# Kernel tuning notes

Hardware: AMD Instinct MI355X
Metric: run time of the kernel (lower is better)

The kernel has to match this reference:

```python
import jax, jax.numpy as jnp
import numpy as np

THRESHOLD = 0.5
N_SEG = 5
NEG_INF = -1e30
EPS = 1e-12  # F.normalize eps


def setup_inputs() -> dict:
    key = jax.random.key(0)
    kx, kl = jax.random.split(key)
    B, D, L = 4096, 512, 80
    x = jax.random.normal(kx, (B, D), dtype=jnp.float32)
    labels = jax.random.randint(kl, (B, L), 0, 2, dtype=jnp.int32)
    return {"x": x, "labels": labels}


def reference(x, labels):
    B = x.shape[0]
    labels_f = labels.astype(jnp.float32)
    # pairwise Jaccard over multi-hot labels
    intersection = labels_f @ labels_f.T                      # [B, B]
    counts = labels_f.sum(axis=1, keepdims=True)              # [B, 1]
    union = counts + counts.T - intersection
    jaccard = intersection / union                            # [B, B]
    # cosine similarity (F.normalize with eps clamp)
    norm = jnp.maximum(jnp.linalg.norm(x, axis=1, keepdims=True), EPS)
    nx = x / norm
    sim = nx @ nx.T                                           # [B, B]
    # --- sample positive (uniform among jaccard > threshold), fixed key ---
    pos_mask = jaccard > THRESHOLD
    valid_mask = jnp.any(pos_mask, axis=1)                    # [B]
    logits = jnp.where(pos_mask, 0.0, NEG_INF)
    sampled = jax.random.categorical(jax.random.key(42), logits, axis=-1)
    pos_samples = jnp.where(valid_mask, sampled, 0)           # invalid rows -> 0
    # --- top-k negatives: jaccard strictly below the positive's jaccard ---
    pos_sim_j = jaccard[jnp.arange(B), pos_samples]           # [B]
    neg_mask = jaccard < pos_sim_j[:, None]
    neg_sims = jnp.where(neg_mask, jaccard, -jnp.inf)
    _, neg_samples = jax.lax.top_k(neg_sims, N_SEG)           # [B, N_SEG]
    # --- contrastive loss on cosine sims at sampled indices ---
    rel_pos = sim[jnp.arange(B), pos_samples]                 # [B]
    rel_neg = jnp.take_along_axis(sim, neg_samples, axis=1)   # [B, N_SEG]
    exp_pos = jnp.exp(rel_pos)
    sum_exp_neg = jnp.exp(rel_neg).sum(axis=1)
    loss = -jnp.log(exp_pos / (exp_pos + sum_exp_neg))
    vm = valid_mask.astype(x.dtype)
    return (loss * vm).sum() / vm.sum()
```

## Files before the change

### kernel.cpp

```cpp
#include <hip/hip_runtime.h>
#include <stdint.h>

#define B_ROWS 4096
#define DIMS   512
#define NLAB   80
#define HALF_ROWS 2048
#define HCNT   8388608u
#define CHUNK  1024
#define SCAP   1024

typedef unsigned long long u64;

__device__ __forceinline__ uint32_t rotl32(uint32_t x, uint32_t d) {
    return (x << d) | (x >> (32u - d));
}

__device__ __forceinline__ void tf2x32_key42(uint32_t c0, uint32_t c1,
                                             uint32_t& o0, uint32_t& o1) {
    const uint32_t ks0 = 0u;
    const uint32_t ks1 = 42u;
    const uint32_t ks2 = 0x1BD11BDAu ^ 0u ^ 42u;
    uint32_t x0 = c0 + ks0;
    uint32_t x1 = c1 + ks1;
#define TF_RND(r) { x0 += x1; x1 = rotl32(x1, (r)); x1 ^= x0; }
    TF_RND(13u) TF_RND(15u) TF_RND(26u) TF_RND(6u)
    x0 += ks1; x1 += ks2 + 1u;
    TF_RND(17u) TF_RND(29u) TF_RND(16u) TF_RND(24u)
    x0 += ks2; x1 += ks0 + 2u;
    TF_RND(13u) TF_RND(15u) TF_RND(26u) TF_RND(6u)
    x0 += ks0; x1 += ks1 + 3u;
    TF_RND(17u) TF_RND(29u) TF_RND(16u) TF_RND(24u)
    x0 += ks1; x1 += ks2 + 4u;
    TF_RND(13u) TF_RND(15u) TF_RND(26u) TF_RND(6u)
    x0 += ks2; x1 += ks0 + 5u;
#undef TF_RND
    o0 = x0; o1 = x1;
}

__device__ __forceinline__ u64 shflx64(u64 v, int m) {
    uint32_t lo = __shfl_xor((uint32_t)(v & 0xFFFFFFFFull), m, 64);
    uint32_t hi = __shfl_xor((uint32_t)(v >> 32), m, 64);
    return ((u64)hi << 32) | (u64)lo;
}

__device__ __forceinline__ uint32_t umx(uint32_t a, uint32_t b) { return a > b ? a : b; }
__device__ __forceinline__ uint32_t umn(uint32_t a, uint32_t b) { return a < b ? a : b; }

__device__ __forceinline__ void ins5_u32(uint32_t* t, uint32_t k) {
    t[4] = umx(t[4], k);
    uint32_t hi, lo;
    hi = umx(t[3], t[4]); lo = umn(t[3], t[4]); t[3] = hi; t[4] = lo;
    hi = umx(t[2], t[3]); lo = umn(t[2], t[3]); t[2] = hi; t[3] = lo;
    hi = umx(t[1], t[2]); lo = umn(t[1], t[2]); t[1] = hi; t[2] = lo;
    hi = umx(t[0], t[1]); lo = umn(t[0], t[1]); t[0] = hi; t[1] = lo;
}

__device__ __forceinline__ void merge5_u32(uint32_t* A, const uint32_t* Bv) {
    uint32_t a0=A[0],a1=A[1],a2=A[2],a3=A[3],a4=A[4];
    uint32_t b0=Bv[0],b1=Bv[1],b2=Bv[2],b3=Bv[3],b4=Bv[4];
    uint32_t m0 = umx(a0, b0);
    uint32_t m1 = umx(umx(a1, b1), umn(a0, b0));
    uint32_t m2 = umx(umx(a2, b2), umx(umn(a0, b1), umn(a1, b0)));
    uint32_t m3 = umx(umx(a3, b3), umx(umx(umn(a0, b2), umn(a1, b1)), umn(a2, b0)));
    uint32_t m4 = umx(umx(a4, b4), umx(umx(umn(a0, b3), umn(a1, b2)),
                                       umx(umn(a2, b1), umn(a3, b0))));
    A[0]=m0; A[1]=m1; A[2]=m2; A[3]=m3; A[4]=m4;
}

__device__ __forceinline__ uint32_t jkey19(uint32_t it, uint32_t u) {
    const uint32_t n = it << 19;
    float f = (float)it * __builtin_amdgcn_rcpf((float)u) * 524288.0f;
    uint32_t ak = (uint32_t)f;
    int r = (int)(n - ak * u);
    if (r < 0) { ak--; r += (int)u; }
    if (r >= (int)u) ak++;
    return ak + 1u;
}


__global__ __launch_bounds__(256) void prep_kernel(const int* __restrict__ labels,
                                                   uint4* __restrict__ pk,
                                                   uint32_t* __restrict__ scnt) {
    const int tid = threadIdx.x;
    const int lane = tid & 63;
    const int row = blockIdx.x * 4 + (tid >> 6);
    const int* lr = labels + (size_t)row * NLAB;
    const int la = lr[lane];
    const int lb = (lane < 16) ? lr[64 + lane] : 0;
    const u64 b0 = __ballot(la != 0);
    const u64 b1 = __ballot(lb != 0);
    const uint32_t w2 = (uint32_t)b1 & 0xFFFFu;
    const uint32_t cnt = (uint32_t)__popcll(b0) + (uint32_t)__popc(w2);
    if (lane == 0) {
        pk[row] = make_uint4((uint32_t)b0, (uint32_t)(b0 >> 32), w2, cnt);
        scnt[row] = 0u;
    }
}

__global__ __launch_bounds__(256) void scan_kernel(const uint4* __restrict__ pk,
                                                   uint32_t* __restrict__ scnt,
                                                   uint32_t* __restrict__ sList,
                                                   uint32_t* __restrict__ keys5P) {
    __shared__ uint4 tab[CHUNK];
    const int tid = threadIdx.x;
    const int grp = (int)blockIdx.x >> 2;
    const int sub = (int)blockIdx.x & 3;
    const int jbase = sub * CHUNK;
#pragma unroll
    for (int k = 0; k < 4; ++k) tab[tid + 256 * k] = pk[jbase + tid + 256 * k];
    __syncthreads();

    const int lane = tid & 63;
    const int pr = grp * 4 + (tid >> 6);
    const int r0 = pr, r1 = pr + HALF_ROWS;
    const uint4 P0 = pk[r0], P1 = pk[r1];
    const uint32_t cw0 = P0.w, cw1 = P1.w;

    uint32_t t0[5], t1[5];
#pragma unroll
    for (int k = 0; k < 5; ++k) {
        const uint32_t fk = (uint32_t)(~(jbase + k)) & 0xFFFu;
        t0[k] = fk; t1[k] = fk;
    }

#pragma unroll 4
    for (int jb = 0; jb < CHUNK; jb += 64) {
        const int jl = jb + lane;
        const int j  = jbase + jl;
        const uint4 pj = tab[jl];
        const uint32_t cj = pj.w;
        const uint32_t jx = (~(uint32_t)j) & 0xFFFu;
        const uint32_t it0 = (uint32_t)(__popc(P0.x & pj.x) + __popc(P0.y & pj.y) + __popc(P0.z & pj.z));
        const uint32_t u0  = cw0 + cj - it0;
        const uint32_t it1 = (uint32_t)(__popc(P1.x & pj.x) + __popc(P1.y & pj.y) + __popc(P1.z & pj.z));
        const uint32_t u1  = cw1 + cj - it1;
        const bool c0 = (it0 << 1) > u0;
        const bool c1 = (it1 << 1) > u1;
        if (__any(c0 || c1)) {
            if (c0) {
                uint32_t slot = atomicAdd(&scnt[r0], 1u);
                if (slot < SCAP) sList[((uint32_t)r0 << 10) + slot] = (it0 << 20) | (u0 << 12) | (uint32_t)j;
            }
            if (c1) {
                uint32_t slot = atomicAdd(&scnt[r1], 1u);
                if (slot < SCAP) sList[((uint32_t)r1 << 10) + slot] = (it1 << 20) | (u1 << 12) | (uint32_t)j;
            }
        }
        if (!c0) {
            const uint32_t thr = umx(t0[4] >> 12, 1u) - 1u;
            if ((it0 << 19) >= __umul24(thr, u0))
                ins5_u32(t0, (jkey19(it0, u0) << 12) | jx);
        }
        if (!c1) {
            const uint32_t thr = umx(t1[4] >> 12, 1u) - 1u;
            if ((it1 << 19) >= __umul24(thr, u1))
                ins5_u32(t1, (jkey19(it1, u1) << 12) | jx);
        }
    }
#pragma unroll
    for (int m = 1; m < 64; m <<= 1) {
        uint32_t o[5];
#pragma unroll
        for (int k = 0; k < 5; ++k) o[k] = __shfl_xor(t0[k], m, 64);
        merge5_u32(t0, o);
#pragma unroll
        for (int k = 0; k < 5; ++k) o[k] = __shfl_xor(t1[k], m, 64);
        merge5_u32(t1, o);
    }
    if (lane == 0) {
        const int idx = (pr << 2) | sub;
#pragma unroll
        for (int k = 0; k < 5; ++k) {
            keys5P[idx * 10 + k]     = t0[k];
            keys5P[idx * 10 + 5 + k] = t1[k];
        }
    }
}

__global__ __launch_bounds__(256) void fin_kernel(const float* __restrict__ x,
                                                  const uint32_t* __restrict__ scnt,
                                                  const uint32_t* __restrict__ sList,
                                                  const uint32_t* __restrict__ keys5P,
                                                  float2* __restrict__ blockPart) {
    __shared__ float lossW[4], cntW[4];
    const int tid = threadIdx.x;
    const int lane = tid & 63;
    const int w = tid >> 6;
    const int row = (int)blockIdx.x * 4 + w;
    const int pr   = row & (HALF_ROWS - 1);
    const int half = row >> 11;

    uint32_t f[5];
#pragma unroll
    for (int k = 0; k < 5; ++k) f[k] = keys5P[((pr << 2) | 0) * 10 + half * 5 + k];
#pragma unroll
    for (int s = 1; s < 4; ++s) {
        uint32_t o[5];
#pragma unroll
        for (int k = 0; k < 5; ++k) o[k] = keys5P[((pr << 2) | s) * 10 + half * 5 + k];
        merge5_u32(f, o);
    }

    const int n = (int)umn(scnt[row], SCAP);
    const uint32_t base23 = (uint32_t)pr * (uint32_t)B_ROWS;
    const uint32_t* sl = sList + ((uint32_t)row << 10);
    u64 gb = 0ull;
    for (int e = lane; e < n; e += 64) {
        const uint32_t ent = sl[e];
        const uint32_t j  = ent & 0xFFFu;
        const uint32_t u  = (ent >> 12) & 0xFFu;
        const uint32_t it = ent >> 20;
        uint32_t o0, o1;
        tf2x32_key42(base23 + j, base23 + j + HCNT, o0, o1);
        const uint32_t o = half ? o1 : o0;
        const u64 key = ((u64)(o >> 9) << 41) | ((u64)((~j) & 0xFFFu) << 29) | (u64)jkey19(it, u);
        if (key > gb) gb = key;
    }
#pragma unroll
    for (int m = 1; m < 64; m <<= 1) {
        const u64 o = shflx64(gb, m);
        if (o > gb) gb = o;
    }
    const bool valid = gb != 0ull;
    const int pos = valid ? (int)((~(uint32_t)(gb >> 29)) & 0xFFFu) : 0;
    const uint32_t pjkey = (uint32_t)(gb & 0xFFFFFu);

    uint32_t ts[5] = {0u, 0u, 0u, 0u, 0u};
    for (int e = lane; e < n; e += 64) {
        const uint32_t ent = sl[e];
        const uint32_t j  = ent & 0xFFFu;
        const uint32_t u  = (ent >> 12) & 0xFFu;
        const uint32_t it = ent >> 20;
        const uint32_t k19 = jkey19(it, u);
        if (k19 < pjkey) ins5_u32(ts, (k19 << 12) | ((~j) & 0xFFFu));
    }
#pragma unroll
    for (int m = 1; m < 64; m <<= 1) {
        uint32_t o[5];
#pragma unroll
        for (int k = 0; k < 5; ++k) o[k] = __shfl_xor(ts[k], m, 64);
        merge5_u32(ts, o);
    }
    merge5_u32(f, ts);

    int tg[6];
    tg[0] = pos;
#pragma unroll
    for (int k = 0; k < 5; ++k) tg[k + 1] = (int)((~f[k]) & 0xFFFu);

    const float* xr = x + (size_t)row * DIMS;
    const float* pp[6];
#pragma unroll
    for (int q = 0; q < 6; ++q) pp[q] = x + (size_t)tg[q] * DIMS;
    float v[8];
#pragma unroll
    for (int u = 0; u < 8; ++u) v[u] = xr[lane + 64 * u];
    float dot[6] = {0.f,0.f,0.f,0.f,0.f,0.f};
    float nsq[6] = {0.f,0.f,0.f,0.f,0.f,0.f};
    float ssq = 0.f;
#pragma unroll
    for (int u = 0; u < 8; ++u) {
        ssq += v[u] * v[u];
#pragma unroll
        for (int q = 0; q < 6; ++q) {
            const float t = pp[q][lane + 64 * u];
            dot[q] += v[u] * t;
            nsq[q] += t * t;
        }
    }
#pragma unroll
    for (int m = 1; m < 64; m <<= 1) {
        ssq += __shfl_xor(ssq, m, 64);
#pragma unroll
        for (int q = 0; q < 6; ++q) {
            dot[q] += __shfl_xor(dot[q], m, 64);
            nsq[q] += __shfl_xor(nsq[q], m, 64);
        }
    }

    if (lane == 0) {
        float loss = 0.f, cnt = 0.f;
        if (valid) {
            const float nr = fmaxf(sqrtf(ssq), 1e-12f);
            const float sp = dot[0] / (nr * fmaxf(sqrtf(nsq[0]), 1e-12f));
            float sen = 0.f;
#pragma unroll
            for (int q = 1; q < 6; ++q)
                sen += expf(dot[q] / (nr * fmaxf(sqrtf(nsq[q]), 1e-12f)));
            const float ep = expf(sp);
            loss = -logf(ep / (ep + sen));
            cnt = 1.f;
        }
        lossW[w] = loss; cntW[w] = cnt;
    }
    __syncthreads();
    if (tid == 0) {
        blockPart[blockIdx.x] = make_float2(lossW[0] + lossW[1] + lossW[2] + lossW[3],
                                            cntW[0] + cntW[1] + cntW[2] + cntW[3]);
    }
}

__global__ __launch_bounds__(256) void final_kernel(const float2* __restrict__ blockPart,
                                                    float* __restrict__ out) {
    __shared__ float rl[4], rc[4];
    const int tid = threadIdx.x;
    const int lane = tid & 63;
    const int w = tid >> 6;
    float sl = 0.f, sc = 0.f;
#pragma unroll
    for (int k = 0; k < 4; ++k) {
        const float2 p = blockPart[tid + 256 * k];
        sl += p.x; sc += p.y;
    }
#pragma unroll
    for (int m = 1; m < 64; m <<= 1) {
        sl += __shfl_xor(sl, m, 64);
        sc += __shfl_xor(sc, m, 64);
    }
    if (lane == 0) { rl[w] = sl; rc[w] = sc; }
    __syncthreads();
    if (tid == 0) out[0] = (rl[0] + rl[1] + rl[2] + rl[3]) / (rc[0] + rc[1] + rc[2] + rc[3]);
}

extern "C" void kernel_launch(void* const* d_in, const int* in_sizes, int n_in,
                              void* d_out, int out_size, void* d_ws, size_t ws_size,
                              hipStream_t stream) {
    const float* x      = (const float*)d_in[0];
    const int*   labels = (const int*)d_in[1];
    float* out = (float*)d_out;

    char* ws = (char*)d_ws;
    uint4*    pk     = (uint4*)ws;
    uint32_t* scnt   = (uint32_t*)(ws + 65536);
    uint32_t* keys5P = (uint32_t*)(ws + 65536 + 16384);
    float2*   bPart  = (float2*)(ws + 65536 + 16384 + 327680);
    uint32_t* sList  = (uint32_t*)(ws + (1u << 20));

    hipLaunchKernelGGL(prep_kernel,  dim3(1024), dim3(256), 0, stream, labels, pk, scnt);
    hipLaunchKernelGGL(scan_kernel,  dim3(2048), dim3(256), 0, stream, pk, scnt, sList, keys5P);
    hipLaunchKernelGGL(fin_kernel,   dim3(1024), dim3(256), 0, stream, x, scnt, sList, keys5P, bPart);
    hipLaunchKernelGGL(final_kernel, dim3(1),    dim3(256), 0, stream, bPart, out);
}
```

Before: 104.1 us.

## Replace per-row atomics with ballot compaction and precompute row norms

The scan kernel drops the global atomicAdd slot allocation. Each wave now compacts its positive candidates with ballot and popcount prefix offsets into a private 256-entry segment per (row, chunk), and writes the per-segment counts at the end. The prep kernel now also computes clamped L2 norms of every x row, so the final kernel only accumulates dot products and reads the stored norms. The row vector load is hoisted to the start of fin_kernel to overlap with the key merging. The trade-off is a per-segment cap of 256 entries, which could overflow for inputs with many positives, plus some duplicated insertion code paths.

```diff
diff --git a/kernel.cpp b/kernel.cpp
--- a/kernel.cpp
+++ b/kernel.cpp
@@ -7,7 +7,7 @@
 #define HALF_ROWS 2048
 #define HCNT   8388608u
 #define CHUNK  1024
-#define SCAP   1024
+#define SEGCAP 256u
 
 typedef unsigned long long u64;
 
@@ -78,9 +78,10 @@
 }
 
 
-__global__ __launch_bounds__(256) void prep_kernel(const int* __restrict__ labels,
+__global__ __launch_bounds__(256) void prep_kernel(const float* __restrict__ x,
+                                                   const int* __restrict__ labels,
                                                    uint4* __restrict__ pk,
-                                                   uint32_t* __restrict__ scnt) {
+                                                   float* __restrict__ norms) {
     const int tid = threadIdx.x;
     const int lane = tid & 63;
     const int row = blockIdx.x * 4 + (tid >> 6);
@@ -91,10 +92,14 @@
     const u64 b1 = __ballot(lb != 0);
     const uint32_t w2 = (uint32_t)b1 & 0xFFFFu;
     const uint32_t cnt = (uint32_t)__popcll(b0) + (uint32_t)__popc(w2);
-    if (lane == 0) {
-        pk[row] = make_uint4((uint32_t)b0, (uint32_t)(b0 >> 32), w2, cnt);
-        scnt[row] = 0u;
-    }
+    if (lane == 0) pk[row] = make_uint4((uint32_t)b0, (uint32_t)(b0 >> 32), w2, cnt);
+    const float* xr = x + (size_t)row * DIMS;
+    float ss = 0.f;
+#pragma unroll
+    for (int u = 0; u < 8; ++u) { float v = xr[lane + 64 * u]; ss += v * v; }
+#pragma unroll
+    for (int m = 1; m < 64; m <<= 1) ss += __shfl_xor(ss, m, 64);
+    if (lane == 0) norms[row] = fmaxf(sqrtf(ss), 1e-12f);
 }
 
 __global__ __launch_bounds__(256) void scan_kernel(const uint4* __restrict__ pk,
@@ -108,13 +113,15 @@
     const int jbase = sub * CHUNK;
 #pragma unroll
     for (int k = 0; k < 4; ++k) tab[tid + 256 * k] = pk[jbase + tid + 256 * k];
-    __syncthreads();
 
     const int lane = tid & 63;
     const int pr = grp * 4 + (tid >> 6);
     const int r0 = pr, r1 = pr + HALF_ROWS;
     const uint4 P0 = pk[r0], P1 = pk[r1];
     const uint32_t cw0 = P0.w, cw1 = P1.w;
+    uint32_t* seg0 = sList + ((((uint32_t)r0 << 2) | sub) << 8);
+    uint32_t* seg1 = sList + ((((uint32_t)r1 << 2) | sub) << 8);
+    uint32_t cnt0 = 0u, cnt1 = 0u;
 
     uint32_t t0[5], t1[5];
 #pragma unroll
@@ -122,6 +129,7 @@
         const uint32_t fk = (uint32_t)(~(jbase + k)) & 0xFFFu;
         t0[k] = fk; t1[k] = fk;
     }
+    __syncthreads();
 
 #pragma unroll 4
     for (int jb = 0; jb < CHUNK; jb += 64) {
@@ -136,26 +144,40 @@
         const uint32_t u1  = cw1 + cj - it1;
         const bool c0 = (it0 << 1) > u0;
         const bool c1 = (it1 << 1) > u1;
-        if (__any(c0 || c1)) {
+        const u64 bal0 = __ballot(c0);
+        const u64 bal1 = __ballot(c1);
+        if (bal0) {
             if (c0) {
-                uint32_t slot = atomicAdd(&scnt[r0], 1u);
-                if (slot < SCAP) sList[((uint32_t)r0 << 10) + slot] = (it0 << 20) | (u0 << 12) | (uint32_t)j;
+                const uint32_t off = cnt0 + (uint32_t)__popcll(bal0 & ((1ull << lane) - 1ull));
+                if (off < SEGCAP) seg0[off] = (it0 << 20) | (u0 << 12) | (uint32_t)j;
             }
-            if (c1) {
-                uint32_t slot = atomicAdd(&scnt[r1], 1u);
-                if (slot < SCAP) sList[((uint32_t)r1 << 10) + slot] = (it1 << 20) | (u1 << 12) | (uint32_t)j;
-            }
-        }
-        if (!c0) {
+            cnt0 += (uint32_t)__popcll(bal0);
+        } else {
             const uint32_t thr = umx(t0[4] >> 12, 1u) - 1u;
             if ((it0 << 19) >= __umul24(thr, u0))
                 ins5_u32(t0, (jkey19(it0, u0) << 12) | jx);
         }
-        if (!c1) {
+        if (!c0 && bal0) {
+            const uint32_t thr = umx(t0[4] >> 12, 1u) - 1u;
+            if ((it0 << 19) >= __umul24(thr, u0))
+                ins5_u32(t0, (jkey19(it0, u0) << 12) | jx);
+        }
+        if (bal1) {
+            if (c1) {
+                const uint32_t off = cnt1 + (uint32_t)__popcll(bal1 & ((1ull << lane) - 1ull));
+                if (off < SEGCAP) seg1[off] = (it1 << 20) | (u1 << 12) | (uint32_t)j;
+            }
+            cnt1 += (uint32_t)__popcll(bal1);
+        } else {
             const uint32_t thr = umx(t1[4] >> 12, 1u) - 1u;
             if ((it1 << 19) >= __umul24(thr, u1))
                 ins5_u32(t1, (jkey19(it1, u1) << 12) | jx);
         }
+        if (!c1 && bal1) {
+            const uint32_t thr = umx(t1[4] >> 12, 1u) - 1u;
+            if ((it1 << 19) >= __umul24(thr, u1))
+                ins5_u32(t1, (jkey19(it1, u1) << 12) | jx);
+        }
     }
 #pragma unroll
     for (int m = 1; m < 64; m <<= 1) {
@@ -168,6 +190,8 @@
         merge5_u32(t1, o);
     }
     if (lane == 0) {
+        scnt[((uint32_t)r0 << 2) | sub] = cnt0;
+        scnt[((uint32_t)r1 << 2) | sub] = cnt1;
         const int idx = (pr << 2) | sub;
 #pragma unroll
         for (int k = 0; k < 5; ++k) {
@@ -178,6 +202,7 @@
 }
 
 __global__ __launch_bounds__(256) void fin_kernel(const float* __restrict__ x,
+                                                  const float* __restrict__ norms,
                                                   const uint32_t* __restrict__ scnt,
                                                   const uint32_t* __restrict__ sList,
                                                   const uint32_t* __restrict__ keys5P,
@@ -189,6 +214,15 @@
     const int row = (int)blockIdx.x * 4 + w;
     const int pr   = row & (HALF_ROWS - 1);
     const int half = row >> 11;
+    const uint32_t rbase = (uint32_t)row << 2;
+
+    const float* xr = x + (size_t)row * DIMS;
+    float v[8];
+#pragma unroll
+    for (int u = 0; u < 8; ++u) v[u] = xr[lane + 64 * u];
+    uint32_t ns[4];
+#pragma unroll
+    for (int s = 0; s < 4; ++s) ns[s] = umn(scnt[rbase + s], SEGCAP);
 
     uint32_t f[5];
 #pragma unroll
@@ -201,20 +235,21 @@
         merge5_u32(f, o);
     }
 
-    const int n = (int)umn(scnt[row], SCAP);
     const uint32_t base23 = (uint32_t)pr * (uint32_t)B_ROWS;
-    const uint32_t* sl = sList + ((uint32_t)row << 10);
     u64 gb = 0ull;
-    for (int e = lane; e < n; e += 64) {
-        const uint32_t ent = sl[e];
-        const uint32_t j  = ent & 0xFFFu;
-        const uint32_t u  = (ent >> 12) & 0xFFu;
-        const uint32_t it = ent >> 20;
-        uint32_t o0, o1;
-        tf2x32_key42(base23 + j, base23 + j + HCNT, o0, o1);
-        const uint32_t o = half ? o1 : o0;
-        const u64 key = ((u64)(o >> 9) << 41) | ((u64)((~j) & 0xFFFu) << 29) | (u64)jkey19(it, u);
-        if (key > gb) gb = key;
+    for (int s = 0; s < 4; ++s) {
+        const uint32_t* sl = sList + ((rbase + s) << 8);
+        for (int e = lane; e < (int)ns[s]; e += 64) {
+            const uint32_t ent = sl[e];
+            const uint32_t j  = ent & 0xFFFu;
+            const uint32_t u  = (ent >> 12) & 0xFFu;
+            const uint32_t it = ent >> 20;
+            uint32_t o0, o1;
+            tf2x32_key42(base23 + j, base23 + j + HCNT, o0, o1);
+            const uint32_t o = half ? o1 : o0;
+            const u64 key = ((u64)(o >> 9) << 41) | ((u64)((~j) & 0xFFFu) << 29) | (u64)jkey19(it, u);
+            if (key > gb) gb = key;
+        }
     }
 #pragma unroll
     for (int m = 1; m < 64; m <<= 1) {
@@ -226,13 +261,16 @@
     const uint32_t pjkey = (uint32_t)(gb & 0xFFFFFu);
 
     uint32_t ts[5] = {0u, 0u, 0u, 0u, 0u};
-    for (int e = lane; e < n; e += 64) {
-        const uint32_t ent = sl[e];
-        const uint32_t j  = ent & 0xFFFu;
-        const uint32_t u  = (ent >> 12) & 0xFFu;
-        const uint32_t it = ent >> 20;
-        const uint32_t k19 = jkey19(it, u);
-        if (k19 < pjkey) ins5_u32(ts, (k19 << 12) | ((~j) & 0xFFFu));
+    for (int s = 0; s < 4; ++s) {
+        const uint32_t* sl = sList + ((rbase + s) << 8);
+        for (int e = lane; e < (int)ns[s]; e += 64) {
+            const uint32_t ent = sl[e];
+            const uint32_t j  = ent & 0xFFFu;
+            const uint32_t u  = (ent >> 12) & 0xFFu;
+            const uint32_t it = ent >> 20;
+            const uint32_t k19 = jkey19(it, u);
+            if (k19 < pjkey) ins5_u32(ts, (k19 << 12) | ((~j) & 0xFFFu));
+        }
     }
 #pragma unroll
     for (int m = 1; m < 64; m <<= 1) {
@@ -248,45 +286,29 @@
 #pragma unroll
     for (int k = 0; k < 5; ++k) tg[k + 1] = (int)((~f[k]) & 0xFFFu);
 
-    const float* xr = x + (size_t)row * DIMS;
     const float* pp[6];
 #pragma unroll
     for (int q = 0; q < 6; ++q) pp[q] = x + (size_t)tg[q] * DIMS;
-    float v[8];
-#pragma unroll
-    for (int u = 0; u < 8; ++u) v[u] = xr[lane + 64 * u];
     float dot[6] = {0.f,0.f,0.f,0.f,0.f,0.f};
-    float nsq[6] = {0.f,0.f,0.f,0.f,0.f,0.f};
-    float ssq = 0.f;
 #pragma unroll
     for (int u = 0; u < 8; ++u) {
-        ssq += v[u] * v[u];
-#pragma unroll
-        for (int q = 0; q < 6; ++q) {
-            const float t = pp[q][lane + 64 * u];
-            dot[q] += v[u] * t;
-            nsq[q] += t * t;
-        }
-    }
-#pragma unroll
-    for (int m = 1; m < 64; m <<= 1) {
-        ssq += __shfl_xor(ssq, m, 64);
-#pragma unroll
-        for (int q = 0; q < 6; ++q) {
-            dot[q] += __shfl_xor(dot[q], m, 64);
-            nsq[q] += __shfl_xor(nsq[q], m, 64);
-        }
+#pragma unroll
+        for (int q = 0; q < 6; ++q) dot[q] += v[u] * pp[q][lane + 64 * u];
+    }
+#pragma unroll
+    for (int m = 1; m < 64; m <<= 1) {
+#pragma unroll
+        for (int q = 0; q < 6; ++q) dot[q] += __shfl_xor(dot[q], m, 64);
     }
 
     if (lane == 0) {
         float loss = 0.f, cnt = 0.f;
         if (valid) {
-            const float nr = fmaxf(sqrtf(ssq), 1e-12f);
-            const float sp = dot[0] / (nr * fmaxf(sqrtf(nsq[0]), 1e-12f));
+            const float nr = norms[row];
+            const float sp = dot[0] / (nr * norms[tg[0]]);
             float sen = 0.f;
 #pragma unroll
-            for (int q = 1; q < 6; ++q)
-                sen += expf(dot[q] / (nr * fmaxf(sqrtf(nsq[q]), 1e-12f)));
+            for (int q = 1; q < 6; ++q) sen += expf(dot[q] / (nr * norms[tg[q]]));
             const float ep = expf(sp);
             loss = -logf(ep / (ep + sen));
             cnt = 1.f;
@@ -331,13 +353,14 @@
 
     char* ws = (char*)d_ws;
     uint4*    pk     = (uint4*)ws;
-    uint32_t* scnt   = (uint32_t*)(ws + 65536);
-    uint32_t* keys5P = (uint32_t*)(ws + 65536 + 16384);
-    float2*   bPart  = (float2*)(ws + 65536 + 16384 + 327680);
+    float*    norms  = (float*)(ws + 65536);
+    uint32_t* scnt   = (uint32_t*)(ws + 65536 + 16384);
+    uint32_t* keys5P = (uint32_t*)(ws + 65536 + 16384 + 65536);
+    float2*   bPart  = (float2*)(ws + 65536 + 16384 + 65536 + 327680);
     uint32_t* sList  = (uint32_t*)(ws + (1u << 20));
 
-    hipLaunchKernelGGL(prep_kernel,  dim3(1024), dim3(256), 0, stream, labels, pk, scnt);
+    hipLaunchKernelGGL(prep_kernel,  dim3(1024), dim3(256), 0, stream, x, labels, pk, norms);
     hipLaunchKernelGGL(scan_kernel,  dim3(2048), dim3(256), 0, stream, pk, scnt, sList, keys5P);
-    hipLaunchKernelGGL(fin_kernel,   dim3(1024), dim3(256), 0, stream, x, scnt, sList, keys5P, bPart);
+    hipLaunchKernelGGL(fin_kernel,   dim3(1024), dim3(256), 0, stream, x, norms, scnt, sList, keys5P, bPart);
     hipLaunchKernelGGL(final_kernel, dim3(1),    dim3(256), 0, stream, bPart, out);
 }
```

Result: faster. 101.4 us (-2.6%).
